# Performance work log

Hardware: AMD Instinct MI355X
Metric: run time of the kernel (lower is better)

Reference implementation:

```python
import jax, jax.numpy as jnp
import numpy as np
import math

N_EMBD = 1024
N_HEAD = 16
HEAD_DIM = N_EMBD // N_HEAD
SCALE = 1.0 / math.sqrt(HEAD_DIM)


def setup_inputs() -> dict:
    key = jax.random.key(0)
    ks = jax.random.split(key, 5)
    B, S = 1, 4096
    std = 0.02
    x = jax.random.normal(ks[0], (B, S, N_EMBD), dtype=jnp.float32)
    # Linear weights stored as [in, out] (transposed vs torch storage; same math)
    w_qkv = jax.random.normal(ks[1], (N_EMBD, 3 * N_EMBD), dtype=jnp.float32) * std
    b_qkv = jnp.zeros((3 * N_EMBD,), dtype=jnp.float32)
    w_out = jax.random.normal(ks[2], (N_EMBD, N_EMBD), dtype=jnp.float32) * std
    b_out = jnp.zeros((N_EMBD,), dtype=jnp.float32)
    return {"x": x, "w_qkv": w_qkv, "b_qkv": b_qkv, "w_out": w_out, "b_out": b_out}


def reference(x, w_qkv, b_qkv, w_out, b_out):
    B, S, D = x.shape
    qkv = x @ w_qkv + b_qkv                      # [B, S, 3D]
    q, k, v = jnp.split(qkv, 3, axis=-1)
    # [B, H, S, d]
    q = q.reshape(B, S, N_HEAD, HEAD_DIM).transpose(0, 2, 1, 3)
    k = k.reshape(B, S, N_HEAD, HEAD_DIM).transpose(0, 2, 1, 3)
    v = v.reshape(B, S, N_HEAD, HEAD_DIM).transpose(0, 2, 1, 3)
    scores = jnp.einsum("bhqd,bhkd->bhqk", q, k) * SCALE  # [B, H, S, S]
    causal = jnp.tril(jnp.ones((S, S), dtype=bool))
    scores = jnp.where(causal, scores, -jnp.inf)
    attn = jax.nn.softmax(scores, axis=-1)
    out = jnp.einsum("bhqk,bhkd->bhqd", attn, v)  # [B, H, S, d]
    out = out.transpose(0, 2, 1, 3).reshape(B, S, D)
    return out @ w_out + b_out
```

## Files before the change

### kernel.cpp

```cpp
#include <hip/hip_runtime.h>
#include <hip/hip_bf16.h>
#include <cstdint>

typedef __bf16 bf16x8 __attribute__((ext_vector_type(8)));
typedef float  f32x4  __attribute__((ext_vector_type(4)));

#define S_LEN 4096
#define D_EMB 1024
#define N3    3072
#define HDIM  64
#define QSCALE 0.180336884f

__device__ __forceinline__ unsigned short f2bf(float f) {
    union { unsigned int i; float f; } v; v.f = f;
    unsigned int i = v.i;
    return (unsigned short)((i + 0x7FFFu + ((i >> 16) & 1u)) >> 16);
}

__device__ __forceinline__ void async16(const void* g, void* l) {
    __builtin_amdgcn_global_load_lds(
        (const __attribute__((address_space(1))) unsigned int*)g,
        (__attribute__((address_space(3))) unsigned int*)l,
        16, 0, 0);
}

__global__ void convert_f32_bf16(const float* __restrict__ src,
                                 unsigned short* __restrict__ dst, int n8) {
    const int i = blockIdx.x * blockDim.x + threadIdx.x;
    if (i >= n8) return;
    float4 f0 = *(const float4*)&src[i * 8];
    float4 f1 = *(const float4*)&src[i * 8 + 4];
    union { uint4 q; unsigned short s[8]; } o;
    o.s[0]=f2bf(f0.x); o.s[1]=f2bf(f0.y); o.s[2]=f2bf(f0.z); o.s[3]=f2bf(f0.w);
    o.s[4]=f2bf(f1.x); o.s[5]=f2bf(f1.y); o.s[6]=f2bf(f1.z); o.s[7]=f2bf(f1.w);
    *(uint4*)&dst[i * 8] = o.q;
}

__global__ void transpose_f32_to_bf16(const float* __restrict__ src,
                                      unsigned short* __restrict__ dst,
                                      int R, int ld, int c0) {
    __shared__ float tile[32][33];
    const int tx = threadIdx.x, ty = threadIdx.y;
    const int r0 = blockIdx.y * 32, cc0 = blockIdx.x * 32;
    for (int i = 0; i < 32; i += 8)
        tile[ty + i][tx] = src[(size_t)(r0 + ty + i) * ld + c0 + cc0 + tx];
    __syncthreads();
    for (int i = 0; i < 32; i += 8)
        dst[(size_t)(cc0 + ty + i) * R + r0 + tx] = f2bf(tile[tx][ty + i]);
}

__global__ void transpose_bf16(const unsigned short* __restrict__ src,
                               unsigned short* __restrict__ dst,
                               int R, int ld, int c0) {
    __shared__ unsigned short tile[32][33];
    const int tx = threadIdx.x, ty = threadIdx.y;
    const int r0 = blockIdx.y * 32, cc0 = blockIdx.x * 32;
    for (int i = 0; i < 32; i += 8)
        tile[ty + i][tx] = src[(size_t)(r0 + ty + i) * ld + c0 + cc0 + tx];
    __syncthreads();
    for (int i = 0; i < 32; i += 8)
        dst[(size_t)(cc0 + ty + i) * R + r0 + tx] = tile[tx][ty + i];
}

template <int MI, bool OUT_F32, bool SCALE_Q>
__global__ __launch_bounds__(256) void gemm_bt_bias(
    const unsigned short* __restrict__ A,
    const unsigned short* __restrict__ BT,
    const float* __restrict__ bias,
    void* __restrict__ Cp,
    int M, int N, int K)
{
    constexpr int MTILE = MI * 32;
    constexpr int LA = MI / 2;
    __shared__ __align__(16) unsigned short As[MTILE * 32];
    __shared__ __align__(16) unsigned short Bs[128 * 32];
    const int tid  = threadIdx.x;
    const int wave = tid >> 6, lane = tid & 63;
    const int q4 = lane >> 4, l16 = lane & 15;
    const int m0 = blockIdx.y * MTILE, n0 = blockIdx.x * 128;
    const int wm = (wave >> 1) * (MI * 16), wn = (wave & 1) * 64;

    f32x4 acc[MI][4] = {};

    const int lrow = lane >> 2;
    const int scol = (lane & 3) * 8;

    for (int k0 = 0; k0 < K; k0 += 32) {
        __syncthreads();
        for (int i = 0; i < 2; ++i) {
            const int r = wave * 32 + i * 16 + lrow;
            async16(BT + (size_t)(n0 + r) * K + k0 + scol,
                    &Bs[(wave * 32 + i * 16) * 32 + lane * 8]);
        }
        for (int i = 0; i < LA; ++i) {
            const int r = wave * (16 * LA) + i * 16 + lrow;
            async16(A + (size_t)(m0 + r) * K + k0 + scol,
                    &As[(wave * (16 * LA) + i * 16) * 32 + lane * 8]);
        }
        __syncthreads();

        bf16x8 af[MI], bfr[4];
        for (int mi = 0; mi < MI; ++mi)
            af[mi] = *(const bf16x8*)&As[(wm + mi * 16 + l16) * 32 + q4 * 8];
        for (int ni = 0; ni < 4; ++ni)
            bfr[ni] = *(const bf16x8*)&Bs[(wn + ni * 16 + l16) * 32 + q4 * 8];
        for (int mi = 0; mi < MI; ++mi)
            for (int ni = 0; ni < 4; ++ni)
                acc[mi][ni] = __builtin_amdgcn_mfma_f32_16x16x32_bf16(
                    af[mi], bfr[ni], acc[mi][ni], 0, 0, 0);
    }

    for (int ni = 0; ni < 4; ++ni) {
        const int col = n0 + wn + ni * 16 + l16;
        const float bv = bias[col];
        const float sc = (SCALE_Q && col < 1024) ? QSCALE : 1.f;
        for (int mi = 0; mi < MI; ++mi) {
            const int row = m0 + wm + mi * 16 + q4 * 4;
            for (int r = 0; r < 4; ++r) {
                const float val = (acc[mi][ni][r] + bv) * sc;
                if constexpr (OUT_F32)
                    ((float*)Cp)[(size_t)(row + r) * N + col] = val;
                else
                    ((unsigned short*)Cp)[(size_t)(row + r) * N + col] = f2bf(val);
            }
        }
    }
}

#define LDP 72
__global__ __launch_bounds__(512) void attn_flash(
    const unsigned short* __restrict__ qkv,
    const unsigned short* __restrict__ Vt,
    unsigned short* __restrict__ X2)
{
    __shared__ __align__(16) unsigned short Ks[64 * LDP];
    __shared__ __align__(16) unsigned short Vs[64 * LDP];
    __shared__ __align__(16) unsigned short Ps[8 * 16 * LDP];
    const int tid  = threadIdx.x;
    const int wave = tid >> 6, lane = tid & 63;
    const int q4 = lane >> 4, l16 = lane & 15;
    const int h  = blockIdx.y;

    const int x = blockIdx.x;
    const int qt = (h < 8) ? x : 31 - x;
    const int q0 = qt * 128;

    bf16x8 aq[2];
    {
        const unsigned short* qp =
            qkv + (size_t)(q0 + wave * 16 + l16) * N3 + h * HDIM + q4 * 8;
        aq[0] = *(const bf16x8*)(qp);
        aq[1] = *(const bf16x8*)(qp + 32);
    }

    float l_part[4] = {0.f, 0.f, 0.f, 0.f};
    f32x4 o[4] = {};

    const int rr = tid >> 3;
    const int cc = (tid & 7) * 8;
    unsigned short* Pw = &Ps[wave * 16 * LDP];
    const int ntile = 2 * qt + 2;

    for (int t = 0; t < ntile; ++t) {
        const int kv0 = t * 64;
        uint4 kv_a = *(const uint4*)&qkv[(size_t)(kv0 + rr) * N3 + D_EMB + h * HDIM + cc];
        uint4 vt_a = *(const uint4*)&Vt [(size_t)(h * HDIM + rr) * S_LEN + kv0 + cc];
        __syncthreads();
        *(uint4*)&Ks[rr * LDP + cc] = kv_a;
        *(uint4*)&Vs[rr * LDP + cc] = vt_a;
        __syncthreads();

        f32x4 sacc[4] = {};
        for (int kk = 0; kk < 2; ++kk)
            for (int nt = 0; nt < 4; ++nt) {
                bf16x8 b = *(const bf16x8*)&Ks[(nt * 16 + l16) * LDP + kk * 32 + q4 * 8];
                sacc[nt] = __builtin_amdgcn_mfma_f32_16x16x32_bf16(
                    aq[kk], b, sacc[nt], 0, 0, 0);
            }

        for (int r = 0; r < 4; ++r) {
            const int grow = q0 + wave * 16 + q4 * 4 + r;
            const int prow = (q4 * 4 + r) * LDP;
            for (int nt = 0; nt < 4; ++nt) {
                float e = exp2f(sacc[nt][r]);
                if (kv0 + nt * 16 + l16 > grow) e = 0.f;
                l_part[r] += e;
                Pw[prow + nt * 16 + l16] =
                    (unsigned short)(__float_as_uint(e) >> 16);
            }
        }
        __asm__ volatile("s_waitcnt lgkmcnt(0)" ::: "memory");

        for (int kk = 0; kk < 2; ++kk) {
            bf16x8 pa = *(const bf16x8*)&Pw[l16 * LDP + kk * 32 + q4 * 8];
            for (int dt = 0; dt < 4; ++dt) {
                bf16x8 vb = *(const bf16x8*)&Vs[(dt * 16 + l16) * LDP + kk * 32 + q4 * 8];
                o[dt] = __builtin_amdgcn_mfma_f32_16x16x32_bf16(pa, vb, o[dt], 0, 0, 0);
            }
        }
    }

    float linv[4];
    for (int r = 0; r < 4; ++r) {
        float l = l_part[r];
        for (int off = 1; off < 16; off <<= 1)
            l += __shfl_xor(l, off, 16);
        linv[r] = 1.f / l;
    }
    for (int dt = 0; dt < 4; ++dt)
        for (int r = 0; r < 4; ++r) {
            const int row = q0 + wave * 16 + q4 * 4 + r;
            X2[(size_t)row * D_EMB + h * HDIM + dt * 16 + l16] =
                f2bf(o[dt][r] * linv[r]);
        }
}

extern "C" void kernel_launch(void* const* d_in, const int* in_sizes, int n_in,
                              void* d_out, int out_size, void* d_ws, size_t ws_size,
                              hipStream_t stream) {
    const float* x     = (const float*)d_in[0];
    const float* w_qkv = (const float*)d_in[1];
    const float* b_qkv = (const float*)d_in[2];
    const float* w_out = (const float*)d_in[3];
    const float* b_out = (const float*)d_in[4];
    float* out = (float*)d_out;

    char* ws = (char*)d_ws;
    unsigned short* qkv   = (unsigned short*)(ws);
    unsigned short* wqkvT = (unsigned short*)(ws + 25165824);
    unsigned short* woutT = (unsigned short*)(ws + 31457280);
    unsigned short* Vt    = (unsigned short*)(ws + 33554432);
    unsigned short* X2    = (unsigned short*)(ws + 41943040);
    unsigned short* Xb    = X2;

    convert_f32_bf16<<<(4096 * 1024 / 8 + 255) / 256, 256, 0, stream>>>(
        x, Xb, 4096 * 1024 / 8);

    transpose_f32_to_bf16<<<dim3(3072 / 32, 1024 / 32), dim3(32, 8), 0, stream>>>(
        w_qkv, wqkvT, 1024, 3072, 0);
    transpose_f32_to_bf16<<<dim3(1024 / 32, 1024 / 32), dim3(32, 8), 0, stream>>>(
        w_out, woutT, 1024, 1024, 0);

    gemm_bt_bias<4, false, true><<<dim3(3072 / 128, 4096 / 128), 256, 0, stream>>>(
        Xb, wqkvT, b_qkv, qkv, 4096, 3072, 1024);

    transpose_bf16<<<dim3(1024 / 32, 4096 / 32), dim3(32, 8), 0, stream>>>(
        qkv, Vt, 4096, 3072, 2048);

    attn_flash<<<dim3(32, 16), 512, 0, stream>>>(qkv, Vt, X2);

    gemm_bt_bias<2, true, false><<<dim3(1024 / 128, 4096 / 64), 256, 0, stream>>>(
        X2, woutT, b_out, out, 4096, 1024, 1024);
}
```

Baseline: 253.8 us.

## Restructure flash attention with split-KV waves, transposed MFMA, and direct global K/V loads

The attention kernel moves to 256-thread blocks over 64-row query tiles. Each block has two wave pairs, and each pair splits the KV tiles between its two waves by parity; partial outputs and row sums are combined through shared memory at the end. K and V fragments are now read straight from global memory instead of being staged in shared memory, which removes the per-tile __syncthreads. Scores are computed transposed so that P can be packed into bf16 pairs and stored as vectors. This aims at better load balance and occupancy and less synchronisation, but it depends on L2/cache bandwidth for K/V reuse and adds a final reduction step.

```diff
diff --git a/kernel.cpp b/kernel.cpp
--- a/kernel.cpp
+++ b/kernel.cpp
@@ -128,91 +128,119 @@
 }
 
 #define LDP 72
-__global__ __launch_bounds__(512) void attn_flash(
+__global__ __launch_bounds__(256, 4) void attn_flash(
     const unsigned short* __restrict__ qkv,
     const unsigned short* __restrict__ Vt,
     unsigned short* __restrict__ X2)
 {
-    __shared__ __align__(16) unsigned short Ks[64 * LDP];
-    __shared__ __align__(16) unsigned short Vs[64 * LDP];
-    __shared__ __align__(16) unsigned short Ps[8 * 16 * LDP];
+    __shared__ __align__(16) unsigned char smem[4 * 32 * LDP * 2];
     const int tid  = threadIdx.x;
     const int wave = tid >> 6, lane = tid & 63;
     const int q4 = lane >> 4, l16 = lane & 15;
     const int h  = blockIdx.y;
-
-    const int x = blockIdx.x;
-    const int qt = (h < 8) ? x : 31 - x;
-    const int q0 = qt * 128;
-
-    bf16x8 aq[2];
-    {
-        const unsigned short* qp =
-            qkv + (size_t)(q0 + wave * 16 + l16) * N3 + h * HDIM + q4 * 8;
-        aq[0] = *(const bf16x8*)(qp);
-        aq[1] = *(const bf16x8*)(qp + 32);
-    }
-
-    float l_part[4] = {0.f, 0.f, 0.f, 0.f};
-    f32x4 o[4] = {};
-
-    const int rr = tid >> 3;
-    const int cc = (tid & 7) * 8;
-    unsigned short* Pw = &Ps[wave * 16 * LDP];
-    const int ntile = 2 * qt + 2;
-
-    for (int t = 0; t < ntile; ++t) {
+    const int wq = wave >> 1, wk = wave & 1;
+
+    const int x = blockIdx.x, hg = blockIdx.y >> 2;
+    int qt;
+    if      (hg == 0) qt = x;
+    else if (hg == 1) qt = 63 - x;
+    else if (hg == 2) qt = (x + 16) & 63;
+    else              qt = (47 - x) & 63;
+    const int q0 = qt * 64;
+
+    unsigned short* Pw = (unsigned short*)(smem + wave * (32 * LDP * 2));
+
+    bf16x8 bq[2][2];
+    for (int mi = 0; mi < 2; ++mi)
+        for (int kk = 0; kk < 2; ++kk)
+            bq[mi][kk] = *(const bf16x8*)&qkv[
+                (size_t)(q0 + wq * 32 + mi * 16 + l16) * N3 + h * HDIM + kk * 32 + q4 * 8];
+
+    f32x4 o[4][2] = {};
+    float l_part[2] = {0.f, 0.f};
+
+    for (int t = wk; t <= qt; t += 2) {
         const int kv0 = t * 64;
-        uint4 kv_a = *(const uint4*)&qkv[(size_t)(kv0 + rr) * N3 + D_EMB + h * HDIM + cc];
-        uint4 vt_a = *(const uint4*)&Vt [(size_t)(h * HDIM + rr) * S_LEN + kv0 + cc];
-        __syncthreads();
-        *(uint4*)&Ks[rr * LDP + cc] = kv_a;
-        *(uint4*)&Vs[rr * LDP + cc] = vt_a;
-        __syncthreads();
-
-        f32x4 sacc[4] = {};
-        for (int kk = 0; kk < 2; ++kk)
-            for (int nt = 0; nt < 4; ++nt) {
-                bf16x8 b = *(const bf16x8*)&Ks[(nt * 16 + l16) * LDP + kk * 32 + q4 * 8];
-                sacc[nt] = __builtin_amdgcn_mfma_f32_16x16x32_bf16(
-                    aq[kk], b, sacc[nt], 0, 0, 0);
-            }
-
-        for (int r = 0; r < 4; ++r) {
-            const int grow = q0 + wave * 16 + q4 * 4 + r;
-            const int prow = (q4 * 4 + r) * LDP;
-            for (int nt = 0; nt < 4; ++nt) {
-                float e = exp2f(sacc[nt][r]);
-                if (kv0 + nt * 16 + l16 > grow) e = 0.f;
-                l_part[r] += e;
-                Pw[prow + nt * 16 + l16] =
-                    (unsigned short)(__float_as_uint(e) >> 16);
+        const bool diag = (t == qt);
+
+        for (int nt = 0; nt < 4; ++nt) {
+            const unsigned short* kp =
+                &qkv[(size_t)(kv0 + nt * 16 + l16) * N3 + D_EMB + h * HDIM + q4 * 8];
+            bf16x8 ak0 = *(const bf16x8*)(kp);
+            bf16x8 ak1 = *(const bf16x8*)(kp + 32);
+            f32x4 s0 = {}, s1 = {};
+            s0 = __builtin_amdgcn_mfma_f32_16x16x32_bf16(ak0, bq[0][0], s0, 0, 0, 0);
+            s1 = __builtin_amdgcn_mfma_f32_16x16x32_bf16(ak0, bq[1][0], s1, 0, 0, 0);
+            s0 = __builtin_amdgcn_mfma_f32_16x16x32_bf16(ak1, bq[0][1], s0, 0, 0, 0);
+            s1 = __builtin_amdgcn_mfma_f32_16x16x32_bf16(ak1, bq[1][1], s1, 0, 0, 0);
+
+            #pragma unroll
+            for (int mi = 0; mi < 2; ++mi) {
+                const f32x4 sv = mi ? s1 : s0;
+                const int qloc = wq * 32 + mi * 16 + l16;
+                unsigned int u[4];
+                #pragma unroll
+                for (int r = 0; r < 4; ++r) {
+                    float e = exp2f(sv[r]);
+                    if (diag && (nt * 16 + q4 * 4 + r > qloc)) e = 0.f;
+                    l_part[mi] += e;
+                    u[r] = __float_as_uint(e);
+                }
+                uint2 pk;
+                pk.x = __builtin_amdgcn_perm(u[1], u[0], 0x07060302u);
+                pk.y = __builtin_amdgcn_perm(u[3], u[2], 0x07060302u);
+                *(uint2*)&Pw[(mi * 16 + l16) * LDP + nt * 16 + q4 * 4] = pk;
             }
         }
         __asm__ volatile("s_waitcnt lgkmcnt(0)" ::: "memory");
 
+        #pragma unroll
         for (int kk = 0; kk < 2; ++kk) {
-            bf16x8 pa = *(const bf16x8*)&Pw[l16 * LDP + kk * 32 + q4 * 8];
-            for (int dt = 0; dt < 4; ++dt) {
-                bf16x8 vb = *(const bf16x8*)&Vs[(dt * 16 + l16) * LDP + kk * 32 + q4 * 8];
-                o[dt] = __builtin_amdgcn_mfma_f32_16x16x32_bf16(pa, vb, o[dt], 0, 0, 0);
-            }
-        }
-    }
-
-    float linv[4];
-    for (int r = 0; r < 4; ++r) {
-        float l = l_part[r];
-        for (int off = 1; off < 16; off <<= 1)
-            l += __shfl_xor(l, off, 16);
-        linv[r] = 1.f / l;
-    }
-    for (int dt = 0; dt < 4; ++dt)
-        for (int r = 0; r < 4; ++r) {
-            const int row = q0 + wave * 16 + q4 * 4 + r;
-            X2[(size_t)row * D_EMB + h * HDIM + dt * 16 + l16] =
-                f2bf(o[dt][r] * linv[r]);
-        }
+            bf16x8 bp0 = *(const bf16x8*)&Pw[(l16)      * LDP + kk * 32 + q4 * 8];
+            bf16x8 bp1 = *(const bf16x8*)&Pw[(16 + l16) * LDP + kk * 32 + q4 * 8];
+            #pragma unroll
+            for (int od = 0; od < 4; ++od) {
+                bf16x8 av = *(const bf16x8*)&Vt[
+                    (size_t)(h * HDIM + od * 16 + l16) * S_LEN + kv0 + kk * 32 + q4 * 8];
+                o[od][0] = __builtin_amdgcn_mfma_f32_16x16x32_bf16(av, bp0, o[od][0], 0, 0, 0);
+                o[od][1] = __builtin_amdgcn_mfma_f32_16x16x32_bf16(av, bp1, o[od][1], 0, 0, 0);
+            }
+        }
+    }
+
+    __syncthreads();
+    float* comb = (float*)(smem + wq * 9216);
+    if (wk == 1) {
+        for (int od = 0; od < 4; ++od)
+            for (int mi = 0; mi < 2; ++mi)
+                *(f32x4*)&comb[lane * 36 + (od * 2 + mi) * 4] = o[od][mi];
+        comb[lane * 36 + 32] = l_part[0];
+        comb[lane * 36 + 33] = l_part[1];
+    }
+    __syncthreads();
+    if (wk == 0) {
+        for (int od = 0; od < 4; ++od)
+            for (int mi = 0; mi < 2; ++mi)
+                o[od][mi] += *(const f32x4*)&comb[lane * 36 + (od * 2 + mi) * 4];
+        l_part[0] += comb[lane * 36 + 32];
+        l_part[1] += comb[lane * 36 + 33];
+        float linv[2];
+        for (int mi = 0; mi < 2; ++mi) {
+            float l = l_part[mi];
+            l += __shfl_xor(l, 16);
+            l += __shfl_xor(l, 32);
+            linv[mi] = 1.f / l;
+        }
+        for (int mi = 0; mi < 2; ++mi) {
+            const int q = q0 + wq * 32 + mi * 16 + l16;
+            for (int od = 0; od < 4; ++od) {
+                union { uint2 u; unsigned short s2[4]; } pk;
+                for (int r = 0; r < 4; ++r)
+                    pk.s2[r] = f2bf(o[od][mi][r] * linv[mi]);
+                *(uint2*)&X2[(size_t)q * D_EMB + h * HDIM + od * 16 + q4 * 4] = pk.u;
+            }
+        }
+    }
 }
 
 extern "C" void kernel_launch(void* const* d_in, const int* in_sizes, int n_in,
@@ -247,7 +275,7 @@
     transpose_bf16<<<dim3(1024 / 32, 4096 / 32), dim3(32, 8), 0, stream>>>(
         qkv, Vt, 4096, 3072, 2048);
 
-    attn_flash<<<dim3(32, 16), 512, 0, stream>>>(qkv, Vt, X2);
+    attn_flash<<<dim3(64, 16), 256, 0, stream>>>(qkv, Vt, X2);
 
     gemm_bt_bias<2, true, false><<<dim3(1024 / 128, 4096 / 64), 256, 0, stream>>>(
         X2, woutT, b_out, out, 4096, 1024, 1024);
```

Result: slower. 305.2 us (+20.2%).
